# Optimization experiments

Measured on AMD Instinct MI355X. Metric: run time of the kernel, lower is better.

Reference implementation:

```python
import jax, jax.numpy as jnp
import numpy as np
import math

B, L, D, H = 16, 144, 512, 8
DH = D // H          # 64, equals structure feature dim
DS, HS = 64, 8       # structure sub-attention model dim / heads
DFF = 2048

def ln(x, g, b, eps=1e-6):
    m = jnp.mean(x, -1, keepdims=True)
    v = jnp.mean((x - m) ** 2, -1, keepdims=True)
    return (x - m) * jax.lax.rsqrt(v + eps) * g + b

def setup_inputs():
    key = jax.random.key(0)
    ks = iter(jax.random.split(key, 32))
    def w(shape, s=0.02):
        return jax.random.normal(next(ks), shape, jnp.float32) * s
    return {
        "inputs": jax.random.normal(next(ks), (B, L, D), jnp.float32),
        "structure": jax.random.normal(next(ks), (L * L, 4, B, DS), jnp.float32),
        "mask": jax.random.randint(next(ks), (B, L, L), 0, 2, jnp.int32),
        "g_att": jnp.ones((D,), jnp.float32), "b_att": jnp.zeros((D,), jnp.float32),
        "Wq": w((D, D)), "bq": jnp.zeros((D,), jnp.float32),
        "Wk": w((D, D)), "bk": jnp.zeros((D,), jnp.float32),
        "Wv": w((D, D)), "bv": jnp.zeros((D,), jnp.float32),
        "Wo": w((D, D)), "bo": jnp.zeros((D,), jnp.float32),
        "sWq": w((DS, DS)), "sbq": jnp.zeros((DS,), jnp.float32),
        "sWk": w((DS, DS)), "sbk": jnp.zeros((DS,), jnp.float32),
        "sWv": w((DS, DS)), "sbv": jnp.zeros((DS,), jnp.float32),
        "sWo": w((DS, DS)), "sbo": jnp.zeros((DS,), jnp.float32),
        "Wc": w((DS, DS, 4)), "bc": jnp.zeros((DS,), jnp.float32),
        "g_s": jnp.ones((DS,), jnp.float32), "b_s": jnp.zeros((DS,), jnp.float32),
        "g_ffn": jnp.ones((D,), jnp.float32), "b_ffn": jnp.zeros((D,), jnp.float32),
        "W1": w((D, DFF)), "b1": jnp.zeros((DFF,), jnp.float32),
        "W2": w((DFF, D)), "b2": jnp.zeros((D,), jnp.float32),
    }

def _forward(inputs, structure, mask, g_att, b_att, Wq, bq, Wk, bk, Wv, bv, Wo, bo,
             sWq, sbq, sWk, sbk, sWv, sbv, sWo, sbo, Wc, bc, g_s, b_s,
             g_ffn, b_ffn, W1, b1, W2, b2):
    x_norm = ln(inputs, g_att, b_att)

    # --- structure pipeline: [L*L,4,B,DS] -> (transpose(0,1),transpose(0,2)) -> [B,L*L,4,DS] -> [N,4,DS]
    N = B * L * L
    s = jnp.transpose(structure, (2, 0, 1, 3)).reshape(N, 4, DS)
    dsh = DS // HS
    def split_s(t):
        return t.reshape(N, 4, HS, dsh).transpose(0, 2, 1, 3)
    q = split_s(s @ sWq + sbq) / math.sqrt(dsh)
    k = split_s(s @ sWk + sbk)
    v = split_s(s @ sWv + sbv)
    attn = jax.nn.softmax(jnp.einsum('nhid,nhjd->nhij', q, k), -1)
    ctx = jnp.einsum('nhij,nhjd->nhid', attn, v).transpose(0, 2, 1, 3).reshape(N, 4, DS)
    sa = ctx @ sWo + sbo                                  # [N,4,DS]
    # Conv1d(64,64,kernel=4) over the length-4 axis (valid -> length 1) + ReLU
    conv = jax.nn.relu(jnp.einsum('ntc,oct->no', sa, Wc) + bc)  # [N,DS]
    R = ln(conv.reshape(B, L, L, DS), g_s, b_s)           # per-pair relation embeddings

    # --- relation-aware self-attention (structure added to keys and values)
    def split_h(t):
        return t.reshape(B, L, H, DH).transpose(0, 2, 1, 3)
    q = split_h(x_norm @ Wq + bq) / math.sqrt(DH)
    k = split_h(x_norm @ Wk + bk)
    v = split_h(x_norm @ Wv + bv)
    scores = jnp.einsum('bhid,bhjd->bhij', q, k) + jnp.einsum('bhid,bijd->bhij', q, R)
    scores = jnp.where(mask[:, None, :, :] != 0, jnp.float32(-1e18), scores)
    attn = jax.nn.softmax(scores, -1)
    ctx = jnp.einsum('bhij,bhjd->bhid', attn, v) + jnp.einsum('bhij,bijd->bhid', attn, R)
    ctx = ctx.transpose(0, 2, 1, 3).reshape(B, L, D)
    x = ctx @ Wo + bo + inputs

    # --- FFN (pre-LN, residual outside)
    h = jax.nn.relu(ln(x, g_ffn, b_ffn) @ W1 + b1)
    return h @ W2 + b2 + x

def reference(inputs, structure, mask, g_att, b_att, Wq, bq, Wk, bk, Wv, bv, Wo, bo,
              sWq, sbq, sWk, sbk, sWv, sbv, sWo, sbo, Wc, bc, g_s, b_s,
              g_ffn, b_ffn, W1, b1, W2, b2):
    return _forward(inputs, structure, mask, g_att, b_att, Wq, bq, Wk, bk, Wv, bv, Wo, bo,
                    sWq, sbq, sWk, sbk, sWv, sbv, sWo, sbo, Wc, bc, g_s, b_s,
                    g_ffn, b_ffn, W1, b1, W2, b2)
```

## Files before the change

kernel.cpp:

```cpp
#include <hip/hip_runtime.h>
#include <math.h>


typedef __bf16 bf16_t;
typedef __bf16 bf16x8 __attribute__((ext_vector_type(8)));
typedef __bf16 bf16x4 __attribute__((ext_vector_type(4)));
typedef __bf16 bf16x2v __attribute__((ext_vector_type(2)));
typedef float f32x4 __attribute__((ext_vector_type(4)));

__global__ __launch_bounds__(256) void transpose_all(
    const float* __restrict__ Wq, const float* __restrict__ Wk,
    const float* __restrict__ Wv, const float* __restrict__ Wo,
    const float* __restrict__ W1, const float* __restrict__ W2,
    bf16_t* __restrict__ WqkvT, bf16_t* __restrict__ WoT,
    bf16_t* __restrict__ W1T, bf16_t* __restrict__ W2T) {
  int bid = blockIdx.x;
  const float* W; bf16_t* WT; int K, N; float scale = 1.f; int tile;
  if (bid < 256)       { W = Wq; WT = WqkvT;            K = 512;  N = 512;  scale = 0.125f; tile = bid; }
  else if (bid < 512)  { W = Wk; WT = WqkvT + 262144;   K = 512;  N = 512;  tile = bid - 256; }
  else if (bid < 768)  { W = Wv; WT = WqkvT + 524288;   K = 512;  N = 512;  tile = bid - 512; }
  else if (bid < 1024) { W = Wo; WT = WoT;              K = 512;  N = 512;  tile = bid - 768; }
  else if (bid < 2048) { W = W1; WT = W1T;              K = 512;  N = 2048; tile = bid - 1024; }
  else                 { W = W2; WT = W2T;              K = 2048; N = 512;  tile = bid - 2048; }
  int ntn = N >> 5;
  int nb = (tile % ntn) * 32, kb = (tile / ntn) * 32;
  __shared__ float t32[32][33];
  int tx = threadIdx.x & 31, ty = threadIdx.x >> 5;
#pragma unroll
  for (int i = ty; i < 32; i += 8) t32[i][tx] = W[(size_t)(kb + i) * N + nb + tx];
  __syncthreads();
#pragma unroll
  for (int i = ty; i < 32; i += 8)
    WT[(size_t)(nb + i) * K + kb + tx] = (__bf16)(t32[tx][i] * scale);
}

__global__ __launch_bounds__(256) void precompute_misc(
    const float* __restrict__ sWq, const float* __restrict__ sWk,
    const float* __restrict__ sWv, const float* __restrict__ sWo,
    const float* __restrict__ sbq, const float* __restrict__ sbk,
    const float* __restrict__ sbv, const float* __restrict__ sbo,
    const float* __restrict__ Wc, const float* __restrict__ bc,
    const float* __restrict__ bq, const float* __restrict__ bk,
    const float* __restrict__ bv, bf16_t* __restrict__ WT3,
    bf16_t* __restrict__ M2T, float* __restrict__ C0,
    float* __restrict__ sbqkv, float* __restrict__ bqkv) {
  int blk = blockIdx.x, tid = threadIdx.x;
  if (blk == 16) {
    const float qs = 0.35355339059327373f;
    for (int idx = tid; idx < 4096; idx += 256) {
      int j = idx >> 6, ic = idx & 63;
      int cj = (j & 7) * 8 + 2 * ((j >> 4) & 3) + ((j >> 3) & 1);
      WT3[idx] = (__bf16)(sWq[ic * 64 + cj] * qs);
      WT3[4096 + idx] = (__bf16)sWk[ic * 64 + cj];
      WT3[8192 + idx] = (__bf16)sWv[ic * 64 + cj];
    }
    if (tid < 64) {
      float s = bc[tid];
      for (int c = 0; c < 64; ++c) {
        float sb = sbo[c];
#pragma unroll
        for (int t = 0; t < 4; ++t) s += sb * Wc[tid * 256 + c * 4 + t];
      }
      C0[tid] = s;
      int cj = (tid & 7) * 8 + 2 * ((tid >> 4) & 3) + ((tid >> 3) & 1);
      sbqkv[tid] = sbq[cj] * qs;
      sbqkv[64 + tid] = sbk[cj];
      sbqkv[128 + tid] = sbv[cj];
    }
  } else if (blk == 17) {
    for (int i = tid; i < 1536; i += 256)
      bqkv[i] = (i < 512) ? bq[i] * 0.125f
                          : ((i < 1024) ? bk[i - 512] : bv[i - 1024]);
  } else {
    int t = blk >> 2;
    int e = (blk & 3) * 16 + (tid >> 4);
    int o4 = (tid & 15) * 4;
    float acc[4] = {0.f, 0.f, 0.f, 0.f};
    for (int c = 0; c < 64; ++c) {
      float a = sWo[e * 64 + c];
#pragma unroll
      for (int j = 0; j < 4; ++j) acc[j] += a * Wc[(o4 + j) * 256 + c * 4 + t];
    }
#pragma unroll
    for (int j = 0; j < 4; ++j)
      M2T[(o4 + j) * 256 + t * 64 + e] = (__bf16)acc[j];
  }
}

__global__ __launch_bounds__(256) void ln512(
    const float* __restrict__ x, const float* __restrict__ g,
    const float* __restrict__ bb, bf16_t* __restrict__ out) {
  int row = blockIdx.x, tid = threadIdx.x;
  const float* xr = x + (size_t)row * 512;
  float2 v = *(const float2*)&xr[tid * 2];
  float s1 = v.x + v.y;
  float s2 = v.x * v.x + v.y * v.y;
#pragma unroll
  for (int m = 32; m >= 1; m >>= 1) {
    s1 += __shfl_xor(s1, m);
    s2 += __shfl_xor(s2, m);
  }
  __shared__ float red[8];
  int wid = tid >> 6;
  if ((tid & 63) == 0) { red[wid * 2] = s1; red[wid * 2 + 1] = s2; }
  __syncthreads();
  s1 = red[0] + red[2] + red[4] + red[6];
  s2 = red[1] + red[3] + red[5] + red[7];
  float mean = s1 * (1.f / 512.f);
  float var = s2 * (1.f / 512.f) - mean * mean;
  float rs = 1.f / sqrtf(var + 1e-6f);
  int c = tid * 2;
  float2 gg = *(const float2*)&g[c];
  float2 bv = *(const float2*)&bb[c];
  bf16x2v o;
  o[0] = (__bf16)((v.x - mean) * rs * gg.x + bv.x);
  o[1] = (__bf16)((v.y - mean) * rs * gg.y + bv.y);
  *(bf16x2v*)&out[(size_t)row * 512 + c] = o;
}

template <int MR>
__global__ __launch_bounds__(256) void gemm_bf16(
    const bf16_t* __restrict__ A, const bf16_t* __restrict__ BT,
    const float* __restrict__ bias, const float* __restrict__ res,
    float* __restrict__ Cf, bf16_t* __restrict__ Cb, int M, int N, int K,
    int relu) {
  constexpr int RT = MR / 64;
  int tid = threadIdx.x;
  int w = tid >> 6, l = tid & 63, l15 = l & 15, l4 = l >> 4;
  int n0 = blockIdx.x * 64, m0 = blockIdx.y * MR;
  const bf16_t* Arow[RT];
#pragma unroll
  for (int rt = 0; rt < RT; ++rt)
    Arow[rt] = A + (size_t)(m0 + (w * RT + rt) * 16 + l15) * K + l4 * 8;
  const bf16_t* Bbase = BT + (size_t)(n0 + l15) * K + l4 * 8;
  f32x4 acc[RT][4];
#pragma unroll
  for (int ct = 0; ct < 4; ++ct) {
    float bv = bias[n0 + ct * 16 + l15];
#pragma unroll
    for (int rt = 0; rt < RT; ++rt) acc[rt][ct] = (f32x4){bv, bv, bv, bv};
  }
#pragma unroll 4
  for (int k0 = 0; k0 < K; k0 += 32) {
    bf16x8 a8[RT];
#pragma unroll
    for (int rt = 0; rt < RT; ++rt) a8[rt] = *(const bf16x8*)(Arow[rt] + k0);
#pragma unroll
    for (int ct = 0; ct < 4; ++ct) {
      bf16x8 b8 = *(const bf16x8*)(Bbase + (size_t)ct * 16 * K + k0);
#pragma unroll
      for (int rt = 0; rt < RT; ++rt)
        acc[rt][ct] =
            __builtin_amdgcn_mfma_f32_16x16x32_bf16(a8[rt], b8, acc[rt][ct], 0, 0, 0);
    }
  }
#pragma unroll
  for (int ct = 0; ct < 4; ++ct) {
    int col = n0 + ct * 16 + l15;
#pragma unroll
    for (int rt = 0; rt < RT; ++rt) {
#pragma unroll
      for (int i = 0; i < 4; ++i) {
        int row = m0 + (w * RT + rt) * 16 + l4 * 4 + i;
        float vv = acc[rt][ct][i];
        if (relu) vv = fmaxf(vv, 0.f);
        if (res) vv += res[(size_t)row * N + col];
        if (Cf) Cf[(size_t)row * N + col] = vv;
        if (Cb) Cb[(size_t)row * N + col] = (__bf16)vv;
      }
    }
  }
}

__global__ __launch_bounds__(256, 2) void struct_mfma(
    const float* __restrict__ S, const bf16_t* __restrict__ WT3,
    const float* __restrict__ sbqkv, const bf16_t* __restrict__ M2T,
    const float* __restrict__ C0, const float* __restrict__ gs,
    const float* __restrict__ bsv, bf16_t* __restrict__ Rout) {
  __shared__ __align__(16) char smem[67584];
  int tid = threadIdx.x;
  int w = tid >> 6, l = tid & 63, l15 = l & 15, l4 = l >> 4;
  int p0 = blockIdx.x * 4;

  bf16x8 wq[4][2], wk[4][2], wv[4][2];
  float biq[4], bik[4], biv[4];
#pragma unroll
  for (int ct = 0; ct < 4; ++ct) {
    int j = ct * 16 + l15;
#pragma unroll
    for (int kb = 0; kb < 2; ++kb) {
      int off = j * 64 + kb * 32 + l4 * 8;
      wq[ct][kb] = *(const bf16x8*)(WT3 + off);
      wk[ct][kb] = *(const bf16x8*)(WT3 + 4096 + off);
      wv[ct][kb] = *(const bf16x8*)(WT3 + 8192 + off);
    }
    biq[ct] = sbqkv[j];
    bik[ct] = sbqkv[64 + j];
    biv[ct] = sbqkv[128 + j];
  }

  {
    int row = tid >> 4;
    int cb0 = (tid & 15) * 16;
    const float* src = S + (size_t)(p0 * 4 + row) * 1024;
    int key = (row & 7) << 4;
#pragma unroll
    for (int i = 0; i < 8; ++i) {
      int colb = cb0 + i * 256;
      int c0 = colb >> 1;
      float4 u0 = *(const float4*)(src + c0);
      float4 u1 = *(const float4*)(src + c0 + 4);
      bf16x8 a;
      a[0] = (__bf16)u0.x; a[1] = (__bf16)u0.y;
      a[2] = (__bf16)u0.z; a[3] = (__bf16)u0.w;
      a[4] = (__bf16)u1.x; a[5] = (__bf16)u1.y;
      a[6] = (__bf16)u1.z; a[7] = (__bf16)u1.w;
      *(bf16x8*)(smem + row * 2048 + (colb ^ key)) = a;
    }
  }
  __syncthreads();

  int pl = l >> 4, h = l & 7, hi = (l >> 3) & 1;
#pragma unroll 1
  for (int r = 0; r < 4; ++r) {
    int b = r * 4 + w;
    int akey = (l15 & 7) << 4;
    int colb0 = b * 128 + l4 * 16;
    bf16x8 af0 = *(const bf16x8*)(smem + l15 * 2048 + (colb0 ^ akey));
    bf16x8 af1 = *(const bf16x8*)(smem + l15 * 2048 + ((colb0 + 64) ^ akey));
    f32x4 aq[4], ak[4], av[4];
#pragma unroll
    for (int ct = 0; ct < 4; ++ct) {
      aq[ct] = (f32x4){biq[ct], biq[ct], biq[ct], biq[ct]};
      ak[ct] = (f32x4){bik[ct], bik[ct], bik[ct], bik[ct]};
      av[ct] = (f32x4){biv[ct], biv[ct], biv[ct], biv[ct]};
    }
#pragma unroll
    for (int ct = 0; ct < 4; ++ct) {
      aq[ct] = __builtin_amdgcn_mfma_f32_16x16x32_bf16(af0, wq[ct][0], aq[ct], 0, 0, 0);
      aq[ct] = __builtin_amdgcn_mfma_f32_16x16x32_bf16(af1, wq[ct][1], aq[ct], 0, 0, 0);
      ak[ct] = __builtin_amdgcn_mfma_f32_16x16x32_bf16(af0, wk[ct][0], ak[ct], 0, 0, 0);
      ak[ct] = __builtin_amdgcn_mfma_f32_16x16x32_bf16(af1, wk[ct][1], ak[ct], 0, 0, 0);
      av[ct] = __builtin_amdgcn_mfma_f32_16x16x32_bf16(af0, wv[ct][0], av[ct], 0, 0, 0);
      av[ct] = __builtin_amdgcn_mfma_f32_16x16x32_bf16(af1, wv[ct][1], av[ct], 0, 0, 0);
    }
    float Sm[4][4];
#pragma unroll
    for (int i2 = 0; i2 < 4; ++i2)
#pragma unroll
      for (int j2 = 0; j2 < 4; ++j2)
        Sm[i2][j2] = aq[0][i2] * ak[0][j2] + aq[1][i2] * ak[1][j2] +
                     aq[2][i2] * ak[2][j2] + aq[3][i2] * ak[3][j2];
#pragma unroll
    for (int i2 = 0; i2 < 4; ++i2)
#pragma unroll
      for (int j2 = 0; j2 < 4; ++j2)
        Sm[i2][j2] += __shfl_xor(Sm[i2][j2], 8);
    float P[4][4], inv[4];
#pragma unroll
    for (int i2 = 0; i2 < 4; ++i2) {
      float rs = 0.f;
#pragma unroll
      for (int j2 = 0; j2 < 4; ++j2) {
        P[i2][j2] = __expf(Sm[i2][j2]);
        rs += P[i2][j2];
      }
      inv[i2] = __builtin_amdgcn_rcpf(rs);
    }
    int unit = r * 16 + w * 4 + pl;
    char* cb = smem + 32768 + unit * 544;
    int ckey = (unit & 7) << 4;
#pragma unroll
    for (int ct = 0; ct < 4; ++ct) {
      int c = h * 8 + 2 * ct + hi;
#pragma unroll
      for (int i2 = 0; i2 < 4; ++i2) {
        float cx = (P[i2][0] * av[ct][0] + P[i2][1] * av[ct][1] +
                    P[i2][2] * av[ct][2] + P[i2][3] * av[ct][3]) * inv[i2];
        *(bf16_t*)(cb + ((i2 * 128 + c * 2) ^ ckey)) = (__bf16)cx;
      }
    }
  }
  __syncthreads();

  float* cvp = (float*)smem;
  {
    bf16x8 ax[8];
    int rkey = (l15 & 7) << 4;
    char* cbase = smem + 32768 + (w * 16 + l15) * 544;
#pragma unroll
    for (int kb = 0; kb < 8; ++kb) {
      int byt = (kb >> 1) * 128 + (kb & 1) * 64 + l4 * 16;
      ax[kb] = *(const bf16x8*)(cbase + (byt ^ rkey));
    }
#pragma unroll 1
    for (int ct = 0; ct < 4; ++ct) {
      int o = ct * 16 + l15;
      float c0v = C0[o];
      f32x4 acc = (f32x4){c0v, c0v, c0v, c0v};
#pragma unroll
      for (int kb = 0; kb < 8; ++kb) {
        bf16x8 mf = *(const bf16x8*)(M2T + o * 256 + kb * 32 + l4 * 8);
        acc = __builtin_amdgcn_mfma_f32_16x16x32_bf16(ax[kb], mf, acc, 0, 0, 0);
      }
#pragma unroll
      for (int i2 = 0; i2 < 4; ++i2)
        cvp[(w * 16 + l4 * 4 + i2) * 68 + o] = fmaxf(acc[i2], 0.f);
    }
  }
  __syncthreads();

  {
    int unit = tid >> 2, ch0 = (tid & 3) * 16;
    const float* cr = cvp + unit * 68 + ch0;
    float4 v0 = *(const float4*)(cr);
    float4 v1 = *(const float4*)(cr + 4);
    float4 v2 = *(const float4*)(cr + 8);
    float4 v3 = *(const float4*)(cr + 12);
    float s1 = v0.x + v0.y + v0.z + v0.w + v1.x + v1.y + v1.z + v1.w +
               v2.x + v2.y + v2.z + v2.w + v3.x + v3.y + v3.z + v3.w;
    float s2 = v0.x * v0.x + v0.y * v0.y + v0.z * v0.z + v0.w * v0.w +
               v1.x * v1.x + v1.y * v1.y + v1.z * v1.z + v1.w * v1.w +
               v2.x * v2.x + v2.y * v2.y + v2.z * v2.z + v2.w * v2.w +
               v3.x * v3.x + v3.y * v3.y + v3.z * v3.z + v3.w * v3.w;
    s1 += __shfl_xor(s1, 1); s1 += __shfl_xor(s1, 2);
    s2 += __shfl_xor(s2, 1); s2 += __shfl_xor(s2, 2);
    float mean = s1 * (1.f / 64.f);
    float var = s2 * (1.f / 64.f) - mean * mean;
    float rstd = 1.f / sqrtf(var + 1e-6f);
    float4 g0 = *(const float4*)&gs[ch0];
    float4 g1 = *(const float4*)&gs[ch0 + 4];
    float4 g2 = *(const float4*)&gs[ch0 + 8];
    float4 g3 = *(const float4*)&gs[ch0 + 12];
    float4 b0 = *(const float4*)&bsv[ch0];
    float4 b1 = *(const float4*)&bsv[ch0 + 4];
    float4 b2 = *(const float4*)&bsv[ch0 + 8];
    float4 b3 = *(const float4*)&bsv[ch0 + 12];
    bf16x8 o0, o1;
    o0[0] = (__bf16)((v0.x - mean) * rstd * g0.x + b0.x);
    o0[1] = (__bf16)((v0.y - mean) * rstd * g0.y + b0.y);
    o0[2] = (__bf16)((v0.z - mean) * rstd * g0.z + b0.z);
    o0[3] = (__bf16)((v0.w - mean) * rstd * g0.w + b0.w);
    o0[4] = (__bf16)((v1.x - mean) * rstd * g1.x + b1.x);
    o0[5] = (__bf16)((v1.y - mean) * rstd * g1.y + b1.y);
    o0[6] = (__bf16)((v1.z - mean) * rstd * g1.z + b1.z);
    o0[7] = (__bf16)((v1.w - mean) * rstd * g1.w + b1.w);
    o1[0] = (__bf16)((v2.x - mean) * rstd * g2.x + b2.x);
    o1[1] = (__bf16)((v2.y - mean) * rstd * g2.y + b2.y);
    o1[2] = (__bf16)((v2.z - mean) * rstd * g2.z + b2.z);
    o1[3] = (__bf16)((v2.w - mean) * rstd * g2.w + b2.w);
    o1[4] = (__bf16)((v3.x - mean) * rstd * g3.x + b3.x);
    o1[5] = (__bf16)((v3.y - mean) * rstd * g3.y + b3.y);
    o1[6] = (__bf16)((v3.z - mean) * rstd * g3.z + b3.z);
    o1[7] = (__bf16)((v3.w - mean) * rstd * g3.w + b3.w);
    int rr = unit >> 4, w2 = (unit >> 2) & 3, pu = unit & 3;
    int b = rr * 4 + w2;
    size_t base = ((size_t)b * 20736 + p0 + pu) * 64 + ch0;
    *(bf16x8*)&Rout[base] = o0;
    *(bf16x8*)&Rout[base + 8] = o1;
  }
}

__global__ __launch_bounds__(256) void attn_main(
    const bf16_t* __restrict__ qkv, const bf16_t* __restrict__ R,
    const int* __restrict__ msk, bf16_t* __restrict__ ctx_out) {
  const int L = 144;
  int blk = blockIdx.x;
  int b = blk / L, i = blk - b * L;
  int tid = threadIdx.x;
  __shared__ float RlT[64][149];
  __shared__ float scl[8][144];
  __shared__ float q8[512];
  const bf16_t* Rrow = R + ((size_t)(b * L + i)) * L * 64;
  for (int idx = tid; idx < 144 * 8; idx += 256) {
    int j = idx >> 3, d8 = (idx & 7) * 8;
    bf16x8 r8 = *(const bf16x8*)&Rrow[(size_t)j * 64 + d8];
#pragma unroll
    for (int e = 0; e < 8; ++e) RlT[d8 + e][j] = (float)r8[e];
  }
  if (tid < 128) {
    bf16x4 q4 = *(const bf16x4*)&qkv[(size_t)(b * L + i) * 1536 + tid * 4];
    float4 qf;
    qf.x = (float)q4[0]; qf.y = (float)q4[1];
    qf.z = (float)q4[2]; qf.w = (float)q4[3];
    *(float4*)&q8[tid * 4] = qf;
  }
  __syncthreads();
  const bf16_t* kb = qkv + (size_t)b * L * 1536 + 512;
  const int* mrow = msk + (size_t)(b * L + i) * 144;
  for (int idx = tid; idx < 8 * 144; idx += 256) {
    int h = idx / 144, j = idx - h * 144;
    const bf16_t* kr = kb + (size_t)j * 1536 + h * 64;
    float s = 0.f;
#pragma unroll
    for (int d0 = 0; d0 < 64; d0 += 8) {
      bf16x8 k8 = *(const bf16x8*)&kr[d0];
      s += q8[h * 64 + d0 + 0] * ((float)k8[0] + RlT[d0 + 0][j]);
      s += q8[h * 64 + d0 + 1] * ((float)k8[1] + RlT[d0 + 1][j]);
      s += q8[h * 64 + d0 + 2] * ((float)k8[2] + RlT[d0 + 2][j]);
      s += q8[h * 64 + d0 + 3] * ((float)k8[3] + RlT[d0 + 3][j]);
      s += q8[h * 64 + d0 + 4] * ((float)k8[4] + RlT[d0 + 4][j]);
      s += q8[h * 64 + d0 + 5] * ((float)k8[5] + RlT[d0 + 5][j]);
      s += q8[h * 64 + d0 + 6] * ((float)k8[6] + RlT[d0 + 6][j]);
      s += q8[h * 64 + d0 + 7] * ((float)k8[7] + RlT[d0 + 7][j]);
    }
    if (mrow[j] != 0) s = -1e18f;
    scl[h][j] = s;
  }
  __syncthreads();
  int h = tid >> 5, l = tid & 31;
  float m = -3.4e38f;
  for (int j = l; j < 144; j += 32) m = fmaxf(m, scl[h][j]);
#pragma unroll
  for (int mm = 16; mm >= 1; mm >>= 1) m = fmaxf(m, __shfl_xor(m, mm));
  float sum = 0.f;
  for (int j = l; j < 144; j += 32) {
    float p = __expf(scl[h][j] - m);
    scl[h][j] = p;
    sum += p;
  }
#pragma unroll
  for (int mm = 16; mm >= 1; mm >>= 1) sum += __shfl_xor(sum, mm);
  float inv = 1.f / sum;
  __syncthreads();
  int d0 = l * 2;
  float a0 = 0.f, a1 = 0.f;
  const bf16_t* vb = qkv + (size_t)b * L * 1536 + 1024 + h * 64 + d0;
  for (int j = 0; j < 144; ++j) {
    float p = scl[h][j];
    bf16x2v vv = *(const bf16x2v*)&vb[(size_t)j * 1536];
    a0 += p * ((float)vv[0] + RlT[d0][j]);
    a1 += p * ((float)vv[1] + RlT[d0 + 1][j]);
  }
  bf16x2v o;
  o[0] = (__bf16)(a0 * inv);
  o[1] = (__bf16)(a1 * inv);
  *(bf16x2v*)&ctx_out[(size_t)(b * L + i) * 512 + h * 64 + d0] = o;
}

extern "C" void kernel_launch(void* const* d_in, const int* in_sizes, int n_in,
                              void* d_out, int out_size, void* d_ws,
                              size_t ws_size, hipStream_t stream) {
  (void)in_sizes; (void)n_in; (void)out_size; (void)ws_size;
  const float* inputs = (const float*)d_in[0];
  const float* structure = (const float*)d_in[1];
  const int* mask = (const int*)d_in[2];
  const float* g_att = (const float*)d_in[3];
  const float* b_att = (const float*)d_in[4];
  const float* Wq = (const float*)d_in[5];
  const float* bq = (const float*)d_in[6];
  const float* Wk = (const float*)d_in[7];
  const float* bk = (const float*)d_in[8];
  const float* Wv = (const float*)d_in[9];
  const float* bv = (const float*)d_in[10];
  const float* Wo = (const float*)d_in[11];
  const float* bo = (const float*)d_in[12];
  const float* sWq = (const float*)d_in[13];
  const float* sbq = (const float*)d_in[14];
  const float* sWk = (const float*)d_in[15];
  const float* sbk = (const float*)d_in[16];
  const float* sWv = (const float*)d_in[17];
  const float* sbv = (const float*)d_in[18];
  const float* sWo = (const float*)d_in[19];
  const float* sbo = (const float*)d_in[20];
  const float* Wc = (const float*)d_in[21];
  const float* bc = (const float*)d_in[22];
  const float* g_s = (const float*)d_in[23];
  const float* b_s = (const float*)d_in[24];
  const float* g_ffn = (const float*)d_in[25];
  const float* b_ffn = (const float*)d_in[26];
  const float* W1 = (const float*)d_in[27];
  const float* b1 = (const float*)d_in[28];
  const float* W2 = (const float*)d_in[29];
  const float* b2 = (const float*)d_in[30];

  char* base = (char*)d_ws;
  bf16_t* Rw = (bf16_t*)base;
  bf16_t* qkvb = (bf16_t*)(base + 42467328);
  float* xw = (float*)(base + 49545216);
  bf16_t* xnb = (bf16_t*)(base + 54263808);
  bf16_t* ctxb = (bf16_t*)(base + 56623104);
  bf16_t* hb = (bf16_t*)(base + 58982400);
  bf16_t* WqkvT = (bf16_t*)(base + 68419584);
  bf16_t* WoT = (bf16_t*)(base + 69992448);
  bf16_t* W1T = (bf16_t*)(base + 70516736);
  bf16_t* W2T = (bf16_t*)(base + 72613888);
  bf16_t* WT3 = (bf16_t*)(base + 74711040);
  bf16_t* M2T = (bf16_t*)(base + 74735616);
  float* C0w = (float*)(base + 74768384);
  float* sbqkv = (float*)(base + 74768640);
  float* bqkv = (float*)(base + 74769408);
  float* out = (float*)d_out;

  transpose_all<<<3072, 256, 0, stream>>>(Wq, Wk, Wv, Wo, W1, W2, WqkvT, WoT,
                                          W1T, W2T);
  precompute_misc<<<18, 256, 0, stream>>>(sWq, sWk, sWv, sWo, sbq, sbk, sbv,
                                          sbo, Wc, bc, bq, bk, bv, WT3, M2T,
                                          C0w, sbqkv, bqkv);
  ln512<<<2304, 256, 0, stream>>>(inputs, g_att, b_att, xnb);
  gemm_bf16<128><<<dim3(24, 18), 256, 0, stream>>>(
      xnb, WqkvT, bqkv, nullptr, nullptr, qkvb, 2304, 1536, 512, 0);
  struct_mfma<<<5184, 256, 0, stream>>>(structure, WT3, sbqkv, M2T, C0w, g_s,
                                        b_s, Rw);
  attn_main<<<2304, 256, 0, stream>>>(qkvb, Rw, mask, ctxb);
  gemm_bf16<64><<<dim3(8, 36), 256, 0, stream>>>(
      ctxb, WoT, bo, inputs, xw, nullptr, 2304, 512, 512, 0);
  ln512<<<2304, 256, 0, stream>>>(xw, g_ffn, b_ffn, xnb);
  gemm_bf16<128><<<dim3(32, 18), 256, 0, stream>>>(
      xnb, W1T, b1, nullptr, nullptr, hb, 2304, 2048, 512, 1);
  gemm_bf16<64><<<dim3(8, 36), 256, 0, stream>>>(
      hb, W2T, b2, xw, out, nullptr, 2304, 512, 2048, 0);
}
```

Measured before the change: 501.5 us.

## Split struct_mfma blocks over batch halves to halve LDS and raise occupancy

Each struct_mfma block now handles only half of the batch dimension (8 of 16 batches) for its 4 positions, so shared memory drops from 66KB to 33KB and launch bounds ask for 4 blocks per CU. The grid doubles, and the final conv and layernorm stages are remapped: two waves share a unit group and split the output channel tiles, and layernorm uses 8 lanes per unit. The aim is more resident waves to hide the latency of the large fp32 structure load. In exchange the per-block weight fragment loads are repeated twice as often, and the tighter register budget may cause spills.

```diff
diff --git a/kernel.cpp b/kernel.cpp
--- a/kernel.cpp
+++ b/kernel.cpp
@@ -172,15 +172,17 @@
   }
 }
 
-__global__ __launch_bounds__(256, 2) void struct_mfma(
+__global__ __launch_bounds__(256, 4) void struct_mfma(
     const float* __restrict__ S, const bf16_t* __restrict__ WT3,
     const float* __restrict__ sbqkv, const bf16_t* __restrict__ M2T,
     const float* __restrict__ C0, const float* __restrict__ gs,
     const float* __restrict__ bsv, bf16_t* __restrict__ Rout) {
-  __shared__ __align__(16) char smem[67584];
+  __shared__ __align__(16) char smem[33792];
   int tid = threadIdx.x;
   int w = tid >> 6, l = tid & 63, l15 = l & 15, l4 = l >> 4;
-  int p0 = blockIdx.x * 4;
+  int bid = blockIdx.x;
+  int p0 = (bid >> 1) * 4;
+  int bgrp = bid & 1;
 
   bf16x8 wq[4][2], wk[4][2], wv[4][2];
   float biq[4], bik[4], biv[4];
@@ -202,10 +204,10 @@
   {
     int row = tid >> 4;
     int cb0 = (tid & 15) * 16;
-    const float* src = S + (size_t)(p0 * 4 + row) * 1024;
+    const float* src = S + (size_t)(p0 * 4 + row) * 1024 + bgrp * 512;
     int key = (row & 7) << 4;
 #pragma unroll
-    for (int i = 0; i < 8; ++i) {
+    for (int i = 0; i < 4; ++i) {
       int colb = cb0 + i * 256;
       int c0 = colb >> 1;
       float4 u0 = *(const float4*)(src + c0);
@@ -215,19 +217,19 @@
       a[2] = (__bf16)u0.z; a[3] = (__bf16)u0.w;
       a[4] = (__bf16)u1.x; a[5] = (__bf16)u1.y;
       a[6] = (__bf16)u1.z; a[7] = (__bf16)u1.w;
-      *(bf16x8*)(smem + row * 2048 + (colb ^ key)) = a;
+      *(bf16x8*)(smem + row * 1024 + (colb ^ key)) = a;
     }
   }
   __syncthreads();
 
   int pl = l >> 4, h = l & 7, hi = (l >> 3) & 1;
 #pragma unroll 1
-  for (int r = 0; r < 4; ++r) {
-    int b = r * 4 + w;
+  for (int r = 0; r < 2; ++r) {
+    int bl = r * 4 + w;
     int akey = (l15 & 7) << 4;
-    int colb0 = b * 128 + l4 * 16;
-    bf16x8 af0 = *(const bf16x8*)(smem + l15 * 2048 + (colb0 ^ akey));
-    bf16x8 af1 = *(const bf16x8*)(smem + l15 * 2048 + ((colb0 + 64) ^ akey));
+    int colb0 = bl * 128 + l4 * 16;
+    bf16x8 af0 = *(const bf16x8*)(smem + l15 * 1024 + (colb0 ^ akey));
+    bf16x8 af1 = *(const bf16x8*)(smem + l15 * 1024 + ((colb0 + 64) ^ akey));
     f32x4 aq[4], ak[4], av[4];
 #pragma unroll
     for (int ct = 0; ct < 4; ++ct) {
@@ -268,7 +270,7 @@
       inv[i2] = __builtin_amdgcn_rcpf(rs);
     }
     int unit = r * 16 + w * 4 + pl;
-    char* cb = smem + 32768 + unit * 544;
+    char* cb = smem + 16384 + unit * 544;
     int ckey = (unit & 7) << 4;
 #pragma unroll
     for (int ct = 0; ct < 4; ++ct) {
@@ -285,16 +287,18 @@
 
   float* cvp = (float*)smem;
   {
+    int ug = w >> 1;
     bf16x8 ax[8];
     int rkey = (l15 & 7) << 4;
-    char* cbase = smem + 32768 + (w * 16 + l15) * 544;
+    char* cbase = smem + 16384 + (ug * 16 + l15) * 544;
 #pragma unroll
     for (int kb = 0; kb < 8; ++kb) {
       int byt = (kb >> 1) * 128 + (kb & 1) * 64 + l4 * 16;
       ax[kb] = *(const bf16x8*)(cbase + (byt ^ rkey));
     }
 #pragma unroll 1
-    for (int ct = 0; ct < 4; ++ct) {
+    for (int cc = 0; cc < 2; ++cc) {
+      int ct = (w & 1) * 2 + cc;
       int o = ct * 16 + l15;
       float c0v = C0[o];
       f32x4 acc = (f32x4){c0v, c0v, c0v, c0v};
@@ -305,59 +309,41 @@
       }
 #pragma unroll
       for (int i2 = 0; i2 < 4; ++i2)
-        cvp[(w * 16 + l4 * 4 + i2) * 68 + o] = fmaxf(acc[i2], 0.f);
+        cvp[(ug * 16 + l4 * 4 + i2) * 68 + o] = fmaxf(acc[i2], 0.f);
     }
   }
   __syncthreads();
 
   {
-    int unit = tid >> 2, ch0 = (tid & 3) * 16;
+    int unit = tid >> 3, ch0 = (tid & 7) * 8;
     const float* cr = cvp + unit * 68 + ch0;
     float4 v0 = *(const float4*)(cr);
     float4 v1 = *(const float4*)(cr + 4);
-    float4 v2 = *(const float4*)(cr + 8);
-    float4 v3 = *(const float4*)(cr + 12);
-    float s1 = v0.x + v0.y + v0.z + v0.w + v1.x + v1.y + v1.z + v1.w +
-               v2.x + v2.y + v2.z + v2.w + v3.x + v3.y + v3.z + v3.w;
+    float s1 = v0.x + v0.y + v0.z + v0.w + v1.x + v1.y + v1.z + v1.w;
     float s2 = v0.x * v0.x + v0.y * v0.y + v0.z * v0.z + v0.w * v0.w +
-               v1.x * v1.x + v1.y * v1.y + v1.z * v1.z + v1.w * v1.w +
-               v2.x * v2.x + v2.y * v2.y + v2.z * v2.z + v2.w * v2.w +
-               v3.x * v3.x + v3.y * v3.y + v3.z * v3.z + v3.w * v3.w;
-    s1 += __shfl_xor(s1, 1); s1 += __shfl_xor(s1, 2);
-    s2 += __shfl_xor(s2, 1); s2 += __shfl_xor(s2, 2);
+               v1.x * v1.x + v1.y * v1.y + v1.z * v1.z + v1.w * v1.w;
+    s1 += __shfl_xor(s1, 1); s1 += __shfl_xor(s1, 2); s1 += __shfl_xor(s1, 4);
+    s2 += __shfl_xor(s2, 1); s2 += __shfl_xor(s2, 2); s2 += __shfl_xor(s2, 4);
     float mean = s1 * (1.f / 64.f);
     float var = s2 * (1.f / 64.f) - mean * mean;
     float rstd = 1.f / sqrtf(var + 1e-6f);
     float4 g0 = *(const float4*)&gs[ch0];
     float4 g1 = *(const float4*)&gs[ch0 + 4];
-    float4 g2 = *(const float4*)&gs[ch0 + 8];
-    float4 g3 = *(const float4*)&gs[ch0 + 12];
     float4 b0 = *(const float4*)&bsv[ch0];
     float4 b1 = *(const float4*)&bsv[ch0 + 4];
-    float4 b2 = *(const float4*)&bsv[ch0 + 8];
-    float4 b3 = *(const float4*)&bsv[ch0 + 12];
-    bf16x8 o0, o1;
-    o0[0] = (__bf16)((v0.x - mean) * rstd * g0.x + b0.x);
-    o0[1] = (__bf16)((v0.y - mean) * rstd * g0.y + b0.y);
-    o0[2] = (__bf16)((v0.z - mean) * rstd * g0.z + b0.z);
-    o0[3] = (__bf16)((v0.w - mean) * rstd * g0.w + b0.w);
-    o0[4] = (__bf16)((v1.x - mean) * rstd * g1.x + b1.x);
-    o0[5] = (__bf16)((v1.y - mean) * rstd * g1.y + b1.y);
-    o0[6] = (__bf16)((v1.z - mean) * rstd * g1.z + b1.z);
-    o0[7] = (__bf16)((v1.w - mean) * rstd * g1.w + b1.w);
-    o1[0] = (__bf16)((v2.x - mean) * rstd * g2.x + b2.x);
-    o1[1] = (__bf16)((v2.y - mean) * rstd * g2.y + b2.y);
-    o1[2] = (__bf16)((v2.z - mean) * rstd * g2.z + b2.z);
-    o1[3] = (__bf16)((v2.w - mean) * rstd * g2.w + b2.w);
-    o1[4] = (__bf16)((v3.x - mean) * rstd * g3.x + b3.x);
-    o1[5] = (__bf16)((v3.y - mean) * rstd * g3.y + b3.y);
-    o1[6] = (__bf16)((v3.z - mean) * rstd * g3.z + b3.z);
-    o1[7] = (__bf16)((v3.w - mean) * rstd * g3.w + b3.w);
-    int rr = unit >> 4, w2 = (unit >> 2) & 3, pu = unit & 3;
-    int b = rr * 4 + w2;
+    bf16x8 ov;
+    ov[0] = (__bf16)((v0.x - mean) * rstd * g0.x + b0.x);
+    ov[1] = (__bf16)((v0.y - mean) * rstd * g0.y + b0.y);
+    ov[2] = (__bf16)((v0.z - mean) * rstd * g0.z + b0.z);
+    ov[3] = (__bf16)((v0.w - mean) * rstd * g0.w + b0.w);
+    ov[4] = (__bf16)((v1.x - mean) * rstd * g1.x + b1.x);
+    ov[5] = (__bf16)((v1.y - mean) * rstd * g1.y + b1.y);
+    ov[6] = (__bf16)((v1.z - mean) * rstd * g1.z + b1.z);
+    ov[7] = (__bf16)((v1.w - mean) * rstd * g1.w + b1.w);
+    int bl = unit >> 2, pu = unit & 3;
+    int b = bgrp * 8 + bl;
     size_t base = ((size_t)b * 20736 + p0 + pu) * 64 + ch0;
-    *(bf16x8*)&Rout[base] = o0;
-    *(bf16x8*)&Rout[base + 8] = o1;
+    *(bf16x8*)&Rout[base] = ov;
   }
 }
 
@@ -500,8 +486,8 @@
   ln512<<<2304, 256, 0, stream>>>(inputs, g_att, b_att, xnb);
   gemm_bf16<128><<<dim3(24, 18), 256, 0, stream>>>(
       xnb, WqkvT, bqkv, nullptr, nullptr, qkvb, 2304, 1536, 512, 0);
-  struct_mfma<<<5184, 256, 0, stream>>>(structure, WT3, sbqkv, M2T, C0w, g_s,
-                                        b_s, Rw);
+  struct_mfma<<<10368, 256, 0, stream>>>(structure, WT3, sbqkv, M2T, C0w, g_s,
+                                         b_s, Rw);
   attn_main<<<2304, 256, 0, stream>>>(qkvb, Rw, mask, ctxb);
   gemm_bf16<64><<<dim3(8, 36), 256, 0, stream>>>(
       ctxb, WoT, bo, inputs, xw, nullptr, 2304, 512, 512, 0);
```

Measured after the change: 832.5 us. 1.66x slower.

## Process two structure tiles per block with register prefetch; read R directly in attention

Applied to the files above, without the earlier changes.

The structure kernel now handles two 4-position tiles per block, halving the grid. The second tile's fp32 input is prefetched into registers while the first tile computes, which overlaps global load latency with MFMA work. Separately, the attention kernel drops its shared-memory transposed copy of R and reads R rows straight from global memory in both the score and context loops. This removes a staging pass and about 38KB of LDS per block, but it adds register pressure from the 16 float4 prefetch buffer and relies on cache hits for the repeated R reads.

```diff
diff --git a/kernel.cpp b/kernel.cpp
--- a/kernel.cpp
+++ b/kernel.cpp
@@ -180,7 +180,7 @@
   __shared__ __align__(16) char smem[67584];
   int tid = threadIdx.x;
   int w = tid >> 6, l = tid & 63, l15 = l & 15, l4 = l >> 4;
-  int p0 = blockIdx.x * 4;
+  int p0 = blockIdx.x * 8;
 
   bf16x8 wq[4][2], wk[4][2], wv[4][2];
   float biq[4], bik[4], biv[4];
@@ -199,14 +199,15 @@
     biv[ct] = sbqkv[128 + j];
   }
 
+  int srow = tid >> 4;
+  int scb0 = (tid & 15) * 16;
+  int skey = (srow & 7) << 4;
+
   {
-    int row = tid >> 4;
-    int cb0 = (tid & 15) * 16;
-    const float* src = S + (size_t)(p0 * 4 + row) * 1024;
-    int key = (row & 7) << 4;
+    const float* src = S + (size_t)(p0 * 4 + srow) * 1024;
 #pragma unroll
     for (int i = 0; i < 8; ++i) {
-      int colb = cb0 + i * 256;
+      int colb = scb0 + i * 256;
       int c0 = colb >> 1;
       float4 u0 = *(const float4*)(src + c0);
       float4 u1 = *(const float4*)(src + c0 + 4);
@@ -215,150 +216,183 @@
       a[2] = (__bf16)u0.z; a[3] = (__bf16)u0.w;
       a[4] = (__bf16)u1.x; a[5] = (__bf16)u1.y;
       a[6] = (__bf16)u1.z; a[7] = (__bf16)u1.w;
-      *(bf16x8*)(smem + row * 2048 + (colb ^ key)) = a;
-    }
-  }
-  __syncthreads();
+      *(bf16x8*)(smem + srow * 2048 + (colb ^ skey)) = a;
+    }
+  }
+  __syncthreads();
+
+  float4 pf[16];
+  {
+    const float* src = S + (size_t)((p0 + 4) * 4 + srow) * 1024;
+#pragma unroll
+    for (int i = 0; i < 8; ++i) {
+      int c0 = (scb0 + i * 256) >> 1;
+      pf[2 * i] = *(const float4*)(src + c0);
+      pf[2 * i + 1] = *(const float4*)(src + c0 + 4);
+    }
+  }
 
   int pl = l >> 4, h = l & 7, hi = (l >> 3) & 1;
+  float* cvp = (float*)smem;
+
+  auto compute_tile = [&](int pt) {
 #pragma unroll 1
-  for (int r = 0; r < 4; ++r) {
-    int b = r * 4 + w;
-    int akey = (l15 & 7) << 4;
-    int colb0 = b * 128 + l4 * 16;
-    bf16x8 af0 = *(const bf16x8*)(smem + l15 * 2048 + (colb0 ^ akey));
-    bf16x8 af1 = *(const bf16x8*)(smem + l15 * 2048 + ((colb0 + 64) ^ akey));
-    f32x4 aq[4], ak[4], av[4];
-#pragma unroll
-    for (int ct = 0; ct < 4; ++ct) {
-      aq[ct] = (f32x4){biq[ct], biq[ct], biq[ct], biq[ct]};
-      ak[ct] = (f32x4){bik[ct], bik[ct], bik[ct], bik[ct]};
-      av[ct] = (f32x4){biv[ct], biv[ct], biv[ct], biv[ct]};
-    }
-#pragma unroll
-    for (int ct = 0; ct < 4; ++ct) {
-      aq[ct] = __builtin_amdgcn_mfma_f32_16x16x32_bf16(af0, wq[ct][0], aq[ct], 0, 0, 0);
-      aq[ct] = __builtin_amdgcn_mfma_f32_16x16x32_bf16(af1, wq[ct][1], aq[ct], 0, 0, 0);
-      ak[ct] = __builtin_amdgcn_mfma_f32_16x16x32_bf16(af0, wk[ct][0], ak[ct], 0, 0, 0);
-      ak[ct] = __builtin_amdgcn_mfma_f32_16x16x32_bf16(af1, wk[ct][1], ak[ct], 0, 0, 0);
-      av[ct] = __builtin_amdgcn_mfma_f32_16x16x32_bf16(af0, wv[ct][0], av[ct], 0, 0, 0);
-      av[ct] = __builtin_amdgcn_mfma_f32_16x16x32_bf16(af1, wv[ct][1], av[ct], 0, 0, 0);
-    }
-    float Sm[4][4];
-#pragma unroll
-    for (int i2 = 0; i2 < 4; ++i2)
-#pragma unroll
-      for (int j2 = 0; j2 < 4; ++j2)
-        Sm[i2][j2] = aq[0][i2] * ak[0][j2] + aq[1][i2] * ak[1][j2] +
-                     aq[2][i2] * ak[2][j2] + aq[3][i2] * ak[3][j2];
-#pragma unroll
-    for (int i2 = 0; i2 < 4; ++i2)
-#pragma unroll
-      for (int j2 = 0; j2 < 4; ++j2)
-        Sm[i2][j2] += __shfl_xor(Sm[i2][j2], 8);
-    float P[4][4], inv[4];
-#pragma unroll
-    for (int i2 = 0; i2 < 4; ++i2) {
-      float rs = 0.f;
-#pragma unroll
-      for (int j2 = 0; j2 < 4; ++j2) {
-        P[i2][j2] = __expf(Sm[i2][j2]);
-        rs += P[i2][j2];
-      }
-      inv[i2] = __builtin_amdgcn_rcpf(rs);
-    }
-    int unit = r * 16 + w * 4 + pl;
-    char* cb = smem + 32768 + unit * 544;
-    int ckey = (unit & 7) << 4;
-#pragma unroll
-    for (int ct = 0; ct < 4; ++ct) {
-      int c = h * 8 + 2 * ct + hi;
+    for (int r = 0; r < 4; ++r) {
+      int b = r * 4 + w;
+      int akey = (l15 & 7) << 4;
+      int colb0 = b * 128 + l4 * 16;
+      bf16x8 af0 = *(const bf16x8*)(smem + l15 * 2048 + (colb0 ^ akey));
+      bf16x8 af1 = *(const bf16x8*)(smem + l15 * 2048 + ((colb0 + 64) ^ akey));
+      f32x4 aq[4], ak[4], av[4];
+#pragma unroll
+      for (int ct = 0; ct < 4; ++ct) {
+        aq[ct] = (f32x4){biq[ct], biq[ct], biq[ct], biq[ct]};
+        ak[ct] = (f32x4){bik[ct], bik[ct], bik[ct], bik[ct]};
+        av[ct] = (f32x4){biv[ct], biv[ct], biv[ct], biv[ct]};
+      }
+#pragma unroll
+      for (int ct = 0; ct < 4; ++ct) {
+        aq[ct] = __builtin_amdgcn_mfma_f32_16x16x32_bf16(af0, wq[ct][0], aq[ct], 0, 0, 0);
+        aq[ct] = __builtin_amdgcn_mfma_f32_16x16x32_bf16(af1, wq[ct][1], aq[ct], 0, 0, 0);
+        ak[ct] = __builtin_amdgcn_mfma_f32_16x16x32_bf16(af0, wk[ct][0], ak[ct], 0, 0, 0);
+        ak[ct] = __builtin_amdgcn_mfma_f32_16x16x32_bf16(af1, wk[ct][1], ak[ct], 0, 0, 0);
+        av[ct] = __builtin_amdgcn_mfma_f32_16x16x32_bf16(af0, wv[ct][0], av[ct], 0, 0, 0);
+        av[ct] = __builtin_amdgcn_mfma_f32_16x16x32_bf16(af1, wv[ct][1], av[ct], 0, 0, 0);
+      }
+      float Sm[4][4];
+#pragma unroll
+      for (int i2 = 0; i2 < 4; ++i2)
+#pragma unroll
+        for (int j2 = 0; j2 < 4; ++j2)
+          Sm[i2][j2] = aq[0][i2] * ak[0][j2] + aq[1][i2] * ak[1][j2] +
+                       aq[2][i2] * ak[2][j2] + aq[3][i2] * ak[3][j2];
+#pragma unroll
+      for (int i2 = 0; i2 < 4; ++i2)
+#pragma unroll
+        for (int j2 = 0; j2 < 4; ++j2)
+          Sm[i2][j2] += __shfl_xor(Sm[i2][j2], 8);
+      float P[4][4], inv[4];
 #pragma unroll
       for (int i2 = 0; i2 < 4; ++i2) {
-        float cx = (P[i2][0] * av[ct][0] + P[i2][1] * av[ct][1] +
-                    P[i2][2] * av[ct][2] + P[i2][3] * av[ct][3]) * inv[i2];
-        *(bf16_t*)(cb + ((i2 * 128 + c * 2) ^ ckey)) = (__bf16)cx;
-      }
-    }
-  }
-  __syncthreads();
-
-  float* cvp = (float*)smem;
+        float rs = 0.f;
+#pragma unroll
+        for (int j2 = 0; j2 < 4; ++j2) {
+          P[i2][j2] = __expf(Sm[i2][j2]);
+          rs += P[i2][j2];
+        }
+        inv[i2] = __builtin_amdgcn_rcpf(rs);
+      }
+      int unit = r * 16 + w * 4 + pl;
+      char* cb = smem + 32768 + unit * 544;
+      int ckey = (unit & 7) << 4;
+#pragma unroll
+      for (int ct = 0; ct < 4; ++ct) {
+        int c = h * 8 + 2 * ct + hi;
+#pragma unroll
+        for (int i2 = 0; i2 < 4; ++i2) {
+          float cx = (P[i2][0] * av[ct][0] + P[i2][1] * av[ct][1] +
+                      P[i2][2] * av[ct][2] + P[i2][3] * av[ct][3]) * inv[i2];
+          *(bf16_t*)(cb + ((i2 * 128 + c * 2) ^ ckey)) = (__bf16)cx;
+        }
+      }
+    }
+    __syncthreads();
+
+    {
+      bf16x8 ax[8];
+      int rkey = (l15 & 7) << 4;
+      char* cbase = smem + 32768 + (w * 16 + l15) * 544;
+#pragma unroll
+      for (int kb = 0; kb < 8; ++kb) {
+        int byt = (kb >> 1) * 128 + (kb & 1) * 64 + l4 * 16;
+        ax[kb] = *(const bf16x8*)(cbase + (byt ^ rkey));
+      }
+#pragma unroll 1
+      for (int ct = 0; ct < 4; ++ct) {
+        int o = ct * 16 + l15;
+        float c0v = C0[o];
+        f32x4 acc = (f32x4){c0v, c0v, c0v, c0v};
+#pragma unroll
+        for (int kb = 0; kb < 8; ++kb) {
+          bf16x8 mf = *(const bf16x8*)(M2T + o * 256 + kb * 32 + l4 * 8);
+          acc = __builtin_amdgcn_mfma_f32_16x16x32_bf16(ax[kb], mf, acc, 0, 0, 0);
+        }
+#pragma unroll
+        for (int i2 = 0; i2 < 4; ++i2)
+          cvp[(w * 16 + l4 * 4 + i2) * 68 + o] = fmaxf(acc[i2], 0.f);
+      }
+    }
+    __syncthreads();
+
+    {
+      int unit = tid >> 2, ch0 = (tid & 3) * 16;
+      const float* cr = cvp + unit * 68 + ch0;
+      float4 v0 = *(const float4*)(cr);
+      float4 v1 = *(const float4*)(cr + 4);
+      float4 v2 = *(const float4*)(cr + 8);
+      float4 v3 = *(const float4*)(cr + 12);
+      float s1 = v0.x + v0.y + v0.z + v0.w + v1.x + v1.y + v1.z + v1.w +
+                 v2.x + v2.y + v2.z + v2.w + v3.x + v3.y + v3.z + v3.w;
+      float s2 = v0.x * v0.x + v0.y * v0.y + v0.z * v0.z + v0.w * v0.w +
+                 v1.x * v1.x + v1.y * v1.y + v1.z * v1.z + v1.w * v1.w +
+                 v2.x * v2.x + v2.y * v2.y + v2.z * v2.z + v2.w * v2.w +
+                 v3.x * v3.x + v3.y * v3.y + v3.z * v3.z + v3.w * v3.w;
+      s1 += __shfl_xor(s1, 1); s1 += __shfl_xor(s1, 2);
+      s2 += __shfl_xor(s2, 1); s2 += __shfl_xor(s2, 2);
+      float mean = s1 * (1.f / 64.f);
+      float var = s2 * (1.f / 64.f) - mean * mean;
+      float rstd = 1.f / sqrtf(var + 1e-6f);
+      float4 g0 = *(const float4*)&gs[ch0];
+      float4 g1 = *(const float4*)&gs[ch0 + 4];
+      float4 g2 = *(const float4*)&gs[ch0 + 8];
+      float4 g3 = *(const float4*)&gs[ch0 + 12];
+      float4 b0 = *(const float4*)&bsv[ch0];
+      float4 b1 = *(const float4*)&bsv[ch0 + 4];
+      float4 b2 = *(const float4*)&bsv[ch0 + 8];
+      float4 b3 = *(const float4*)&bsv[ch0 + 12];
+      bf16x8 o0, o1;
+      o0[0] = (__bf16)((v0.x - mean) * rstd * g0.x + b0.x);
+      o0[1] = (__bf16)((v0.y - mean) * rstd * g0.y + b0.y);
+      o0[2] = (__bf16)((v0.z - mean) * rstd * g0.z + b0.z);
+      o0[3] = (__bf16)((v0.w - mean) * rstd * g0.w + b0.w);
+      o0[4] = (__bf16)((v1.x - mean) * rstd * g1.x + b1.x);
+      o0[5] = (__bf16)((v1.y - mean) * rstd * g1.y + b1.y);
+      o0[6] = (__bf16)((v1.z - mean) * rstd * g1.z + b1.z);
+      o0[7] = (__bf16)((v1.w - mean) * rstd * g1.w + b1.w);
+      o1[0] = (__bf16)((v2.x - mean) * rstd * g2.x + b2.x);
+      o1[1] = (__bf16)((v2.y - mean) * rstd * g2.y + b2.y);
+      o1[2] = (__bf16)((v2.z - mean) * rstd * g2.z + b2.z);
+      o1[3] = (__bf16)((v2.w - mean) * rstd * g2.w + b2.w);
+      o1[4] = (__bf16)((v3.x - mean) * rstd * g3.x + b3.x);
+      o1[5] = (__bf16)((v3.y - mean) * rstd * g3.y + b3.y);
+      o1[6] = (__bf16)((v3.z - mean) * rstd * g3.z + b3.z);
+      o1[7] = (__bf16)((v3.w - mean) * rstd * g3.w + b3.w);
+      int rr = unit >> 4, w2 = (unit >> 2) & 3, pu = unit & 3;
+      int b = rr * 4 + w2;
+      size_t base = ((size_t)b * 20736 + pt + pu) * 64 + ch0;
+      *(bf16x8*)&Rout[base] = o0;
+      *(bf16x8*)&Rout[base + 8] = o1;
+    }
+  };
+
+  compute_tile(p0);
+  __syncthreads();
+
   {
-    bf16x8 ax[8];
-    int rkey = (l15 & 7) << 4;
-    char* cbase = smem + 32768 + (w * 16 + l15) * 544;
-#pragma unroll
-    for (int kb = 0; kb < 8; ++kb) {
-      int byt = (kb >> 1) * 128 + (kb & 1) * 64 + l4 * 16;
-      ax[kb] = *(const bf16x8*)(cbase + (byt ^ rkey));
-    }
-#pragma unroll 1
-    for (int ct = 0; ct < 4; ++ct) {
-      int o = ct * 16 + l15;
-      float c0v = C0[o];
-      f32x4 acc = (f32x4){c0v, c0v, c0v, c0v};
-#pragma unroll
-      for (int kb = 0; kb < 8; ++kb) {
-        bf16x8 mf = *(const bf16x8*)(M2T + o * 256 + kb * 32 + l4 * 8);
-        acc = __builtin_amdgcn_mfma_f32_16x16x32_bf16(ax[kb], mf, acc, 0, 0, 0);
-      }
-#pragma unroll
-      for (int i2 = 0; i2 < 4; ++i2)
-        cvp[(w * 16 + l4 * 4 + i2) * 68 + o] = fmaxf(acc[i2], 0.f);
-    }
-  }
-  __syncthreads();
-
-  {
-    int unit = tid >> 2, ch0 = (tid & 3) * 16;
-    const float* cr = cvp + unit * 68 + ch0;
-    float4 v0 = *(const float4*)(cr);
-    float4 v1 = *(const float4*)(cr + 4);
-    float4 v2 = *(const float4*)(cr + 8);
-    float4 v3 = *(const float4*)(cr + 12);
-    float s1 = v0.x + v0.y + v0.z + v0.w + v1.x + v1.y + v1.z + v1.w +
-               v2.x + v2.y + v2.z + v2.w + v3.x + v3.y + v3.z + v3.w;
-    float s2 = v0.x * v0.x + v0.y * v0.y + v0.z * v0.z + v0.w * v0.w +
-               v1.x * v1.x + v1.y * v1.y + v1.z * v1.z + v1.w * v1.w +
-               v2.x * v2.x + v2.y * v2.y + v2.z * v2.z + v2.w * v2.w +
-               v3.x * v3.x + v3.y * v3.y + v3.z * v3.z + v3.w * v3.w;
-    s1 += __shfl_xor(s1, 1); s1 += __shfl_xor(s1, 2);
-    s2 += __shfl_xor(s2, 1); s2 += __shfl_xor(s2, 2);
-    float mean = s1 * (1.f / 64.f);
-    float var = s2 * (1.f / 64.f) - mean * mean;
-    float rstd = 1.f / sqrtf(var + 1e-6f);
-    float4 g0 = *(const float4*)&gs[ch0];
-    float4 g1 = *(const float4*)&gs[ch0 + 4];
-    float4 g2 = *(const float4*)&gs[ch0 + 8];
-    float4 g3 = *(const float4*)&gs[ch0 + 12];
-    float4 b0 = *(const float4*)&bsv[ch0];
-    float4 b1 = *(const float4*)&bsv[ch0 + 4];
-    float4 b2 = *(const float4*)&bsv[ch0 + 8];
-    float4 b3 = *(const float4*)&bsv[ch0 + 12];
-    bf16x8 o0, o1;
-    o0[0] = (__bf16)((v0.x - mean) * rstd * g0.x + b0.x);
-    o0[1] = (__bf16)((v0.y - mean) * rstd * g0.y + b0.y);
-    o0[2] = (__bf16)((v0.z - mean) * rstd * g0.z + b0.z);
-    o0[3] = (__bf16)((v0.w - mean) * rstd * g0.w + b0.w);
-    o0[4] = (__bf16)((v1.x - mean) * rstd * g1.x + b1.x);
-    o0[5] = (__bf16)((v1.y - mean) * rstd * g1.y + b1.y);
-    o0[6] = (__bf16)((v1.z - mean) * rstd * g1.z + b1.z);
-    o0[7] = (__bf16)((v1.w - mean) * rstd * g1.w + b1.w);
-    o1[0] = (__bf16)((v2.x - mean) * rstd * g2.x + b2.x);
-    o1[1] = (__bf16)((v2.y - mean) * rstd * g2.y + b2.y);
-    o1[2] = (__bf16)((v2.z - mean) * rstd * g2.z + b2.z);
-    o1[3] = (__bf16)((v2.w - mean) * rstd * g2.w + b2.w);
-    o1[4] = (__bf16)((v3.x - mean) * rstd * g3.x + b3.x);
-    o1[5] = (__bf16)((v3.y - mean) * rstd * g3.y + b3.y);
-    o1[6] = (__bf16)((v3.z - mean) * rstd * g3.z + b3.z);
-    o1[7] = (__bf16)((v3.w - mean) * rstd * g3.w + b3.w);
-    int rr = unit >> 4, w2 = (unit >> 2) & 3, pu = unit & 3;
-    int b = rr * 4 + w2;
-    size_t base = ((size_t)b * 20736 + p0 + pu) * 64 + ch0;
-    *(bf16x8*)&Rout[base] = o0;
-    *(bf16x8*)&Rout[base + 8] = o1;
-  }
+#pragma unroll
+    for (int i = 0; i < 8; ++i) {
+      int colb = scb0 + i * 256;
+      float4 u0 = pf[2 * i], u1 = pf[2 * i + 1];
+      bf16x8 a;
+      a[0] = (__bf16)u0.x; a[1] = (__bf16)u0.y;
+      a[2] = (__bf16)u0.z; a[3] = (__bf16)u0.w;
+      a[4] = (__bf16)u1.x; a[5] = (__bf16)u1.y;
+      a[6] = (__bf16)u1.z; a[7] = (__bf16)u1.w;
+      *(bf16x8*)(smem + srow * 2048 + (colb ^ skey)) = a;
+    }
+  }
+  __syncthreads();
+  compute_tile(p0 + 4);
 }
 
 __global__ __launch_bounds__(256) void attn_main(
@@ -368,16 +402,9 @@
   int blk = blockIdx.x;
   int b = blk / L, i = blk - b * L;
   int tid = threadIdx.x;
-  __shared__ float RlT[64][149];
   __shared__ float scl[8][144];
   __shared__ float q8[512];
   const bf16_t* Rrow = R + ((size_t)(b * L + i)) * L * 64;
-  for (int idx = tid; idx < 144 * 8; idx += 256) {
-    int j = idx >> 3, d8 = (idx & 7) * 8;
-    bf16x8 r8 = *(const bf16x8*)&Rrow[(size_t)j * 64 + d8];
-#pragma unroll
-    for (int e = 0; e < 8; ++e) RlT[d8 + e][j] = (float)r8[e];
-  }
   if (tid < 128) {
     bf16x4 q4 = *(const bf16x4*)&qkv[(size_t)(b * L + i) * 1536 + tid * 4];
     float4 qf;
@@ -391,18 +418,20 @@
   for (int idx = tid; idx < 8 * 144; idx += 256) {
     int h = idx / 144, j = idx - h * 144;
     const bf16_t* kr = kb + (size_t)j * 1536 + h * 64;
+    const bf16_t* rr = Rrow + (size_t)j * 64;
     float s = 0.f;
 #pragma unroll
     for (int d0 = 0; d0 < 64; d0 += 8) {
       bf16x8 k8 = *(const bf16x8*)&kr[d0];
-      s += q8[h * 64 + d0 + 0] * ((float)k8[0] + RlT[d0 + 0][j]);
-      s += q8[h * 64 + d0 + 1] * ((float)k8[1] + RlT[d0 + 1][j]);
-      s += q8[h * 64 + d0 + 2] * ((float)k8[2] + RlT[d0 + 2][j]);
-      s += q8[h * 64 + d0 + 3] * ((float)k8[3] + RlT[d0 + 3][j]);
-      s += q8[h * 64 + d0 + 4] * ((float)k8[4] + RlT[d0 + 4][j]);
-      s += q8[h * 64 + d0 + 5] * ((float)k8[5] + RlT[d0 + 5][j]);
-      s += q8[h * 64 + d0 + 6] * ((float)k8[6] + RlT[d0 + 6][j]);
-      s += q8[h * 64 + d0 + 7] * ((float)k8[7] + RlT[d0 + 7][j]);
+      bf16x8 r8 = *(const bf16x8*)&rr[d0];
+      s += q8[h * 64 + d0 + 0] * ((float)k8[0] + (float)r8[0]);
+      s += q8[h * 64 + d0 + 1] * ((float)k8[1] + (float)r8[1]);
+      s += q8[h * 64 + d0 + 2] * ((float)k8[2] + (float)r8[2]);
+      s += q8[h * 64 + d0 + 3] * ((float)k8[3] + (float)r8[3]);
+      s += q8[h * 64 + d0 + 4] * ((float)k8[4] + (float)r8[4]);
+      s += q8[h * 64 + d0 + 5] * ((float)k8[5] + (float)r8[5]);
+      s += q8[h * 64 + d0 + 6] * ((float)k8[6] + (float)r8[6]);
+      s += q8[h * 64 + d0 + 7] * ((float)k8[7] + (float)r8[7]);
     }
     if (mrow[j] != 0) s = -1e18f;
     scl[h][j] = s;
@@ -426,11 +455,13 @@
   int d0 = l * 2;
   float a0 = 0.f, a1 = 0.f;
   const bf16_t* vb = qkv + (size_t)b * L * 1536 + 1024 + h * 64 + d0;
+  const bf16_t* rb = Rrow + d0;
   for (int j = 0; j < 144; ++j) {
     float p = scl[h][j];
     bf16x2v vv = *(const bf16x2v*)&vb[(size_t)j * 1536];
-    a0 += p * ((float)vv[0] + RlT[d0][j]);
-    a1 += p * ((float)vv[1] + RlT[d0 + 1][j]);
+    bf16x2v rv = *(const bf16x2v*)&rb[(size_t)j * 64];
+    a0 += p * ((float)vv[0] + (float)rv[0]);
+    a1 += p * ((float)vv[1] + (float)rv[1]);
   }
   bf16x2v o;
   o[0] = (__bf16)(a0 * inv);
@@ -500,7 +531,7 @@
   ln512<<<2304, 256, 0, stream>>>(inputs, g_att, b_att, xnb);
   gemm_bf16<128><<<dim3(24, 18), 256, 0, stream>>>(
       xnb, WqkvT, bqkv, nullptr, nullptr, qkvb, 2304, 1536, 512, 0);
-  struct_mfma<<<5184, 256, 0, stream>>>(structure, WT3, sbqkv, M2T, C0w, g_s,
+  struct_mfma<<<2592, 256, 0, stream>>>(structure, WT3, sbqkv, M2T, C0w, g_s,
                                         b_s, Rw);
   attn_main<<<2304, 256, 0, stream>>>(qkvb, Rw, mask, ctxb);
   gemm_bf16<64><<<dim3(8, 36), 256, 0, stream>>>(
```

New measurement: 663.6 us. 1.32x slower.
